# Performance work log

Measured on AMD Instinct MI355X. Metric: run time of the kernel, lower is better.

Reference implementation:

```python
import jax, jax.numpy as jnp
import numpy as np

B, CIN, COUT, G = 1, 64, 64, 1
NLAT, NLON = 256, 512
LMAX, MMAX = NLAT, NLON // 2 + 1  # torch-harmonics: lmax=nlat, mmax=nlon//2+1


def _legpoly(mmax, lmax, cost):
    """Fully (ortho) normalized associated Legendre \bar P_l^m(cos t), shape [mmax, lmax, nlat]."""
    nlat = cost.shape[0]
    p = np.zeros((mmax, lmax, nlat), dtype=np.float64)
    sint = np.sqrt(1.0 - cost * cost)
    pmm = np.full(nlat, np.sqrt(1.0 / (4.0 * np.pi)))  # \bar P_0^0
    for m in range(mmax):
        if m < lmax:
            p[m, m] = pmm
        if m + 1 < lmax:
            p[m, m + 1] = np.sqrt(2.0 * m + 3.0) * cost * pmm
        for l in range(m + 2, lmax):
            a = np.sqrt((4.0 * l * l - 1.0) / (l * l - m * m))
            b = np.sqrt(((l - 1.0) ** 2 - m * m) / (4.0 * (l - 1.0) ** 2 - 1.0))
            p[m, l] = a * (cost * p[m, l - 1] - b * p[m, l - 2])
        # diagonal step: \bar P_{m+1}^{m+1}
        pmm = -np.sqrt((2.0 * m + 3.0) / (2.0 * m + 2.0)) * sint * pmm
    return p


def setup_inputs():
    key = jax.random.key(0)
    k1, k2, k3 = jax.random.split(key, 3)
    # Gauss-Legendre nodes/weights (grid='legendre-gauss')
    cost, wq = np.polynomial.legendre.leggauss(NLAT)
    pct = _legpoly(MMAX, LMAX, cost)                      # [m, l, k] - ISHT matrix
    sht_w = pct * wq[None, None, :]                        # [m, l, k] - SHT matrix (Legendre * quadrature)
    x = jax.random.normal(k1, (B, CIN, NLAT, NLON), jnp.float32)
    # weight init: scale = sqrt(1/(Cin/g)), scale[0] *= sqrt(2); complex randn has var 1/2 per component
    scale = np.full(LMAX, np.sqrt(1.0 / (CIN // G)), np.float32)
    scale[0] *= np.sqrt(2.0)
    scale = scale * np.sqrt(0.5)
    weight_r = jax.random.normal(k2, (G, CIN // G, COUT // G, LMAX), jnp.float32) * scale
    weight_i = jax.random.normal(k3, (G, CIN // G, COUT // G, LMAX), jnp.float32) * scale
    return {"x": x, "weight_r": weight_r, "weight_i": weight_i,
            "pct": jnp.asarray(pct.astype(np.float32)),
            "sht_w": jnp.asarray(sht_w.astype(np.float32))}


def reference(x, weight_r, weight_i, pct, sht_w):
    residual = x  # scale_residual is False (same in/out shape and grid)
    x = x.astype(jnp.float32)
    # --- forward real SHT: rfft over lon, Legendre transform over lat ---
    xf = 2.0 * jnp.pi * jnp.fft.rfft(x, axis=-1, norm="forward")          # [B,C,k,m] complex64
    coeffs = jnp.einsum('bckm,mlk->bclm', xf, sht_w.astype(xf.dtype))      # [B,C,l,m]
    Bd, C, L, M = coeffs.shape
    # --- grouped per-l complex weight contraction (_contract_lwise) ---
    w = (weight_r + 1j * weight_i).astype(coeffs.dtype)                    # [g,i,o,l]
    xg = coeffs.reshape(Bd, G, C // G, L, M)
    out = jnp.einsum('bgilm,giol->bgolm', xg, w).reshape(Bd, COUT, L, M)
    # --- inverse real SHT ---
    xk = jnp.einsum('bolm,mlk->bokm', out, pct.astype(out.dtype))          # [B,Cout,k,m]
    y = jnp.fft.irfft(xk, n=NLON, axis=-1, norm="forward")                 # [B,Cout,nlat,nlon]
    return (y.astype(residual.dtype), residual)
```

## Files before the change

kernel.cpp:

```cpp
#include <hip/hip_runtime.h>

typedef _Float16 f16;
typedef _Float16 h8 __attribute__((ext_vector_type(8)));
typedef float f4 __attribute__((ext_vector_type(4)));

#define NLON 512
#define NLAT 256
#define NC   64
#define NM   256
#define NL   256
#define RTOT (NC*NLAT)

#define BO_FTR 0
#define BO_FTI (BO_FTR + 262144)
#define BO_GR  (BO_FTI + 262144)
#define BO_GI  (BO_GR  + 262144)
#define BO_WTR (BO_GI  + 262144)
#define BO_WTI (BO_WTR + 2097152)
#define BO_XFRE (BO_WTI + 2097152)
#define BO_XFIM (BO_XFRE + 8388608)
#define BO_PRE  (BO_XFIM + 8388608)
#define BO_PIM  (BO_PRE + 8388608)
#define BO_QRE  (BO_PIM + 8388608)
#define BO_QIM  (BO_QRE + 8388608)

__device__ inline f4 mfma16(h8 a, h8 b, f4 c) {
  return __builtin_amdgcn_mfma_f32_16x16x32_f16(a, b, c, 0, 0, 0);
}

__global__ void k_tables_h(f16* __restrict__ Ftr, f16* __restrict__ Fti,
                           f16* __restrict__ Gr, f16* __restrict__ Gi) {
  int idx = blockIdx.x * blockDim.x + threadIdx.x;
  if (idx >= NLON * NM) return;
  const float step = 3.14159265358979323846f / 256.0f;
  {
    int m = idx >> 9, n = idx & 511;
    int t = (n * m) & (NLON - 1);
    float th = t * step;
    const float sc = 6.2831853071795864769f / 512.0f;
    Ftr[idx] = (f16)(sc * cosf(th));
    Fti[idx] = (f16)(-sc * sinf(th));
  }
  {
    int n = idx >> 8, m = idx & 255;
    int t = (n * m) & (NLON - 1);
    float th = t * step;
    float s = (m == 0) ? 1.0f : 2.0f;
    Gr[idx] = (f16)(s * cosf(th));
    Gi[idx] = (f16)(-s * sinf(th));
  }
}

__global__ void k_permw2(const float* __restrict__ wr, const float* __restrict__ wi,
                         f16* __restrict__ wTr, f16* __restrict__ wTi) {
  __shared__ float tile[32][33];
  int z = blockIdx.z;
  int o = z >> 1;
  const float* w = (z & 1) ? wi : wr;
  f16* wT = (z & 1) ? wTi : wTr;
  int i0 = blockIdx.y * 32;
  int l0 = blockIdx.x * 32;
  int xx = threadIdx.x, yy = threadIdx.y;
  for (int j = 0; j < 32; j += 8)
    tile[yy + j][xx] = w[(size_t)(i0 + yy + j) * (NC * NL) + (size_t)o * NL + l0 + xx];
  __syncthreads();
  for (int j = 0; j < 32; j += 8)
    wT[(size_t)(l0 + yy + j) * (NC * NC) + (size_t)o * NC + i0 + xx] = (f16)tile[xx][yy + j];
}

__global__ __launch_bounds__(256) void k_s1(
    const float* __restrict__ x, const f16* __restrict__ Ftr,
    const f16* __restrict__ Fti, f16* __restrict__ XFre, f16* __restrict__ XFim,
    float* __restrict__ res) {
  __shared__ f16 Ar[64 * 40], Ai[64 * 40], Bx[64 * 40];
  int t = threadIdx.x;
  int m0 = blockIdx.x * 64, r0 = blockIdx.y * 64;
  int lane = t & 63, w = t >> 6;
  int wm = (w >> 1) * 32, wn = (w & 1) * 32;
  int fr = lane & 15, kg = (lane >> 4) * 8;
  int srow = t >> 2, skc = (t & 3) * 8;
  f4 aR[2][2] = {}, aI[2][2] = {};
  for (int n0 = 0; n0 < NLON; n0 += 32) {
    *(h8*)&Ar[srow * 40 + skc] = *(const h8*)(Ftr + (size_t)(m0 + srow) * NLON + n0 + skc);
    *(h8*)&Ai[srow * 40 + skc] = *(const h8*)(Fti + (size_t)(m0 + srow) * NLON + n0 + skc);
    const float* px = x + (size_t)(r0 + srow) * NLON + n0 + skc;
    float4 v0 = *(const float4*)px;
    float4 v1 = *(const float4*)(px + 4);
    if (blockIdx.x == 0) {
      float* pr = res + (size_t)(r0 + srow) * NLON + n0 + skc;
      *(float4*)pr = v0;
      *(float4*)(pr + 4) = v1;
    }
    h8 hx = {(f16)v0.x, (f16)v0.y, (f16)v0.z, (f16)v0.w,
             (f16)v1.x, (f16)v1.y, (f16)v1.z, (f16)v1.w};
    *(h8*)&Bx[srow * 40 + skc] = hx;
    __syncthreads();
    h8 a0 = *(h8*)&Ar[(wm + fr) * 40 + kg];
    h8 a1 = *(h8*)&Ar[(wm + 16 + fr) * 40 + kg];
    h8 c0 = *(h8*)&Ai[(wm + fr) * 40 + kg];
    h8 c1 = *(h8*)&Ai[(wm + 16 + fr) * 40 + kg];
    h8 b0 = *(h8*)&Bx[(wn + fr) * 40 + kg];
    h8 b1 = *(h8*)&Bx[(wn + 16 + fr) * 40 + kg];
    aR[0][0] = mfma16(a0, b0, aR[0][0]); aR[0][1] = mfma16(a0, b1, aR[0][1]);
    aR[1][0] = mfma16(a1, b0, aR[1][0]); aR[1][1] = mfma16(a1, b1, aR[1][1]);
    aI[0][0] = mfma16(c0, b0, aI[0][0]); aI[0][1] = mfma16(c0, b1, aI[0][1]);
    aI[1][0] = mfma16(c1, b0, aI[1][0]); aI[1][1] = mfma16(c1, b1, aI[1][1]);
    __syncthreads();
  }
  int drow = (lane >> 4) * 4, dcol = lane & 15;
#pragma unroll
  for (int i = 0; i < 2; ++i)
#pragma unroll
    for (int j = 0; j < 2; ++j)
#pragma unroll
      for (int b = 0; b < 4; ++b) {
        size_t o = (size_t)(m0 + wm + i * 16 + drow + b) * RTOT + r0 + wn + j * 16 + dcol;
        XFre[o] = (f16)aR[i][j][b];
        XFim[o] = (f16)aI[i][j][b];
      }
}

__global__ __launch_bounds__(256) void k_s2(
    const f16* __restrict__ XFre, const f16* __restrict__ XFim,
    const float* __restrict__ shtw, f16* __restrict__ Pre, f16* __restrict__ Pim) {
  int m = blockIdx.y;
  int l0 = blockIdx.x * 64;
  int t = threadIdx.x;
  if (l0 + 64 <= m) {
    h8 z = {};
#pragma unroll
    for (int rep = 0; rep < 2; ++rep) {
      int f = rep * 256 + t;
      int ll = f >> 3, c8 = (f & 7) * 8;
      size_t o = (size_t)(l0 + ll) * RTOT + (size_t)m * 64 + c8;
      *(h8*)(Pre + o) = z;
      *(h8*)(Pim + o) = z;
    }
    return;
  }
  __shared__ f16 SH[9216];
  f16* Ar = SH;
  f16* Ai = SH + 2560;
  f16* Bs = SH + 5120;
  int lane = t & 63, w = t >> 6;
  int wm = (w >> 1) * 32, wn = (w & 1) * 32;
  int fr = lane & 15, kg = (lane >> 4) * 8;
  int srow = t >> 2, skc = (t & 3) * 8;
  const f16* Abr = XFre + (size_t)m * RTOT;
  const f16* Abi = XFim + (size_t)m * RTOT;
  const float* Bb = shtw + (size_t)m * (NL * NLAT);
  f4 aR[2][2] = {}, aI[2][2] = {};
  for (int k0 = 0; k0 < NLAT; k0 += 32) {
    *(h8*)&Ar[srow * 40 + skc] = *(const h8*)(Abr + (size_t)srow * NLAT + k0 + skc);
    *(h8*)&Ai[srow * 40 + skc] = *(const h8*)(Abi + (size_t)srow * NLAT + k0 + skc);
    const float* pb = Bb + (size_t)(l0 + srow) * NLAT + k0 + skc;
    float4 v0 = *(const float4*)pb;
    float4 v1 = *(const float4*)(pb + 4);
    h8 hb = {(f16)v0.x, (f16)v0.y, (f16)v0.z, (f16)v0.w,
             (f16)v1.x, (f16)v1.y, (f16)v1.z, (f16)v1.w};
    *(h8*)&Bs[srow * 40 + skc] = hb;
    __syncthreads();
    h8 a0 = *(h8*)&Ar[(wm + fr) * 40 + kg],      a1 = *(h8*)&Ar[(wm + 16 + fr) * 40 + kg];
    h8 c0 = *(h8*)&Ai[(wm + fr) * 40 + kg],      c1 = *(h8*)&Ai[(wm + 16 + fr) * 40 + kg];
    h8 b0 = *(h8*)&Bs[(wn + fr) * 40 + kg],      b1 = *(h8*)&Bs[(wn + 16 + fr) * 40 + kg];
    aR[0][0] = mfma16(a0, b0, aR[0][0]); aR[0][1] = mfma16(a0, b1, aR[0][1]);
    aR[1][0] = mfma16(a1, b0, aR[1][0]); aR[1][1] = mfma16(a1, b1, aR[1][1]);
    aI[0][0] = mfma16(c0, b0, aI[0][0]); aI[0][1] = mfma16(c0, b1, aI[0][1]);
    aI[1][0] = mfma16(c1, b0, aI[1][0]); aI[1][1] = mfma16(c1, b1, aI[1][1]);
    __syncthreads();
  }
  f16* Tr = SH;
  f16* Ti = SH + 4608;
  int drow = (lane >> 4) * 4, dcol = lane & 15;
#pragma unroll
  for (int i = 0; i < 2; ++i)
#pragma unroll
    for (int j = 0; j < 2; ++j)
#pragma unroll
      for (int b = 0; b < 4; ++b) {
        int c = wm + i * 16 + drow + b;
        int l = wn + j * 16 + dcol;
        Tr[l * 72 + c] = (f16)aR[i][j][b];
        Ti[l * 72 + c] = (f16)aI[i][j][b];
      }
  __syncthreads();
#pragma unroll
  for (int rep = 0; rep < 4; ++rep) {
    int f = rep * 256 + t;
    int buf = f >> 9, idx = f & 511;
    int ll = idx >> 3, c8 = (idx & 7) * 8;
    const f16* T = buf ? Ti : Tr;
    h8 v = *(const h8*)&T[ll * 72 + c8];
    f16* Pd = buf ? Pim : Pre;
    *(h8*)(Pd + (size_t)(l0 + ll) * RTOT + (size_t)m * 64 + c8) = v;
  }
}

__global__ __launch_bounds__(256) void k_s3(
    const f16* __restrict__ Pre, const f16* __restrict__ Pim,
    const f16* __restrict__ wTr, const f16* __restrict__ wTi,
    f16* __restrict__ Qre, f16* __restrict__ Qim) {
  int l = blockIdx.y;
  int m0 = blockIdx.x * 64;
  int t = threadIdx.x;
  size_t obase = (size_t)l * RTOT + (size_t)m0 * 64;
  if (m0 > l) {
    h8 z = {};
#pragma unroll
    for (int rep = 0; rep < 2; ++rep) {
      int f = rep * 256 + t;
      ((h8*)(Qre + obase))[f] = z;
      ((h8*)(Qim + obase))[f] = z;
    }
    return;
  }
  __shared__ f16 SH[18432];
  f16* Ar = SH;
  f16* Ai = SH + 4608;
  f16* Br = SH + 9216;
  f16* Bi = SH + 13824;
  const f16* Pbr = Pre + (size_t)l * RTOT + (size_t)m0 * 64;
  const f16* Pbi = Pim + (size_t)l * RTOT + (size_t)m0 * 64;
  const f16* Wbr = wTr + (size_t)l * 4096;
  const f16* Wbi = wTi + (size_t)l * 4096;
#pragma unroll
  for (int rep = 0; rep < 2; ++rep) {
    int f = rep * 256 + t;
    int row = f >> 3, c8 = (f & 7) * 8;
    *(h8*)&Ar[row * 72 + c8] = *(const h8*)(Pbr + (size_t)row * 64 + c8);
    *(h8*)&Ai[row * 72 + c8] = *(const h8*)(Pbi + (size_t)row * 64 + c8);
    *(h8*)&Br[row * 72 + c8] = *(const h8*)(Wbr + (size_t)f * 8);
    *(h8*)&Bi[row * 72 + c8] = *(const h8*)(Wbi + (size_t)f * 8);
  }
  __syncthreads();
  int lane = t & 63, w = t >> 6;
  int wm = (w >> 1) * 32, wn = (w & 1) * 32;
  int fr = lane & 15, kg = (lane >> 4) * 8;
  f4 RR[2][2] = {}, II[2][2] = {}, RI[2][2] = {}, IR[2][2] = {};
#pragma unroll
  for (int ks = 0; ks < 64; ks += 32) {
    h8 a0 = *(h8*)&Ar[(wm + fr) * 72 + ks + kg];
    h8 a1 = *(h8*)&Ar[(wm + 16 + fr) * 72 + ks + kg];
    h8 c0 = *(h8*)&Ai[(wm + fr) * 72 + ks + kg];
    h8 c1 = *(h8*)&Ai[(wm + 16 + fr) * 72 + ks + kg];
    h8 b0 = *(h8*)&Br[(wn + fr) * 72 + ks + kg];
    h8 b1 = *(h8*)&Br[(wn + 16 + fr) * 72 + ks + kg];
    h8 d0 = *(h8*)&Bi[(wn + fr) * 72 + ks + kg];
    h8 d1 = *(h8*)&Bi[(wn + 16 + fr) * 72 + ks + kg];
    RR[0][0] = mfma16(a0, b0, RR[0][0]); RR[0][1] = mfma16(a0, b1, RR[0][1]);
    RR[1][0] = mfma16(a1, b0, RR[1][0]); RR[1][1] = mfma16(a1, b1, RR[1][1]);
    II[0][0] = mfma16(c0, d0, II[0][0]); II[0][1] = mfma16(c0, d1, II[0][1]);
    II[1][0] = mfma16(c1, d0, II[1][0]); II[1][1] = mfma16(c1, d1, II[1][1]);
    RI[0][0] = mfma16(a0, d0, RI[0][0]); RI[0][1] = mfma16(a0, d1, RI[0][1]);
    RI[1][0] = mfma16(a1, d0, RI[1][0]); RI[1][1] = mfma16(a1, d1, RI[1][1]);
    IR[0][0] = mfma16(c0, b0, IR[0][0]); IR[0][1] = mfma16(c0, b1, IR[0][1]);
    IR[1][0] = mfma16(c1, b0, IR[1][0]); IR[1][1] = mfma16(c1, b1, IR[1][1]);
  }
  __syncthreads();
  f16* Tr = SH;
  f16* Ti = SH + 4608;
  int drow = (lane >> 4) * 4, dcol = lane & 15;
#pragma unroll
  for (int i = 0; i < 2; ++i)
#pragma unroll
    for (int j = 0; j < 2; ++j)
#pragma unroll
      for (int b = 0; b < 4; ++b) {
        int mm = wm + i * 16 + drow + b;
        int oo = wn + j * 16 + dcol;
        Tr[mm * 72 + oo] = (f16)(RR[i][j][b] - II[i][j][b]);
        Ti[mm * 72 + oo] = (f16)(RI[i][j][b] + IR[i][j][b]);
      }
  __syncthreads();
#pragma unroll
  for (int rep = 0; rep < 4; ++rep) {
    int f = rep * 256 + t;
    int buf = f >> 9, idx = f & 511;
    int mm = idx >> 3, o8 = (idx & 7) * 8;
    const f16* T = buf ? Ti : Tr;
    h8 v = *(const h8*)&T[mm * 72 + o8];
    f16* Qd = buf ? Qim : Qre;
    *(h8*)(Qd + obase + (size_t)mm * 64 + o8) = v;
  }
}

__global__ __launch_bounds__(256) void k_s4(
    const f16* __restrict__ Qre, const f16* __restrict__ Qim,
    const float* __restrict__ pct, f16* __restrict__ XKre, f16* __restrict__ XKim) {
  __shared__ f16 As[32 * 66], Ais[32 * 66], Bs0[32 * 66], Bs1[32 * 66];
  int m = blockIdx.y;
  int k0b = blockIdx.x * 128;
  int t = threadIdx.x;
  int lane = t & 63, w = t >> 6;
  int wm = (w >> 1) * 32, wn = (w & 1) * 32;
  int fr = lane & 15, kg = (lane >> 4) * 8;
  int lr = t >> 3, c8 = (t & 7) * 8;
  const float* Bb = pct + (size_t)m * (NL * NLAT);
  f4 aR[2][4] = {}, aI[2][4] = {};
  int lstart = m & ~31;
  for (int l0 = lstart; l0 < NL; l0 += 32) {
    *(h8*)&As[lr * 66 + c8]  = *(const h8*)(Qre + (size_t)(l0 + lr) * RTOT + (size_t)m * 64 + c8);
    *(h8*)&Ais[lr * 66 + c8] = *(const h8*)(Qim + (size_t)(l0 + lr) * RTOT + (size_t)m * 64 + c8);
    const float* pb = Bb + (size_t)(l0 + lr) * NLAT + k0b + c8;
    {
      float4 v0 = *(const float4*)pb;
      float4 v1 = *(const float4*)(pb + 4);
      h8 hb = {(f16)v0.x, (f16)v0.y, (f16)v0.z, (f16)v0.w,
               (f16)v1.x, (f16)v1.y, (f16)v1.z, (f16)v1.w};
      *(h8*)&Bs0[lr * 66 + c8] = hb;
    }
    {
      float4 v0 = *(const float4*)(pb + 64);
      float4 v1 = *(const float4*)(pb + 68);
      h8 hb = {(f16)v0.x, (f16)v0.y, (f16)v0.z, (f16)v0.w,
               (f16)v1.x, (f16)v1.y, (f16)v1.z, (f16)v1.w};
      *(h8*)&Bs1[lr * 66 + c8] = hb;
    }
    __syncthreads();
    h8 a0, a1, c0, c1, b0, b1, b2, b3;
#pragma unroll
    for (int e = 0; e < 8; ++e) {
      int row = (kg + e) * 66;
      a0[e] = As[row + wm + fr];
      a1[e] = As[row + wm + 16 + fr];
      c0[e] = Ais[row + wm + fr];
      c1[e] = Ais[row + wm + 16 + fr];
      b0[e] = Bs0[row + wn + fr];
      b1[e] = Bs0[row + wn + 16 + fr];
      b2[e] = Bs1[row + wn + fr];
      b3[e] = Bs1[row + wn + 16 + fr];
    }
    aR[0][0] = mfma16(a0, b0, aR[0][0]); aR[0][1] = mfma16(a0, b1, aR[0][1]);
    aR[0][2] = mfma16(a0, b2, aR[0][2]); aR[0][3] = mfma16(a0, b3, aR[0][3]);
    aR[1][0] = mfma16(a1, b0, aR[1][0]); aR[1][1] = mfma16(a1, b1, aR[1][1]);
    aR[1][2] = mfma16(a1, b2, aR[1][2]); aR[1][3] = mfma16(a1, b3, aR[1][3]);
    aI[0][0] = mfma16(c0, b0, aI[0][0]); aI[0][1] = mfma16(c0, b1, aI[0][1]);
    aI[0][2] = mfma16(c0, b2, aI[0][2]); aI[0][3] = mfma16(c0, b3, aI[0][3]);
    aI[1][0] = mfma16(c1, b0, aI[1][0]); aI[1][1] = mfma16(c1, b1, aI[1][1]);
    aI[1][2] = mfma16(c1, b2, aI[1][2]); aI[1][3] = mfma16(c1, b3, aI[1][3]);
    __syncthreads();
  }
  int drow = (lane >> 4) * 4, dcol = lane & 15;
#pragma unroll
  for (int i = 0; i < 2; ++i)
#pragma unroll
    for (int j = 0; j < 4; ++j)
#pragma unroll
      for (int b = 0; b < 4; ++b) {
        int orow = wm + i * 16 + drow + b;
        int kcol = k0b + (j >> 1) * 64 + (j & 1) * 16 + wn + dcol;
        size_t o = (size_t)m * RTOT + (size_t)orow * NLAT + kcol;
        XKre[o] = (f16)aR[i][j][b];
        XKim[o] = (f16)aI[i][j][b];
      }
}

__global__ __launch_bounds__(256) void k_s5(
    const f16* __restrict__ XKre, const f16* __restrict__ XKim,
    const f16* __restrict__ Gr, const f16* __restrict__ Gi,
    float* __restrict__ y) {
  __shared__ f16 Ar[32 * 66], Ai[32 * 66], Br[128 * 34], Bi[128 * 34];
  int t = threadIdx.x;
  int n0 = blockIdx.x * 128, r0 = blockIdx.y * 64;
  int lane = t & 63, w = t >> 6;
  int wm = (w >> 1) * 32, wn = (w & 1) * 32;
  int fr = lane & 15, kg = (lane >> 4) * 8;
  int mr = t >> 3, r8 = (t & 7) * 8;
  f4 acc[2][4] = {};
  for (int m0 = 0; m0 < NM; m0 += 32) {
    *(h8*)&Ar[mr * 66 + r8] = *(const h8*)(XKre + (size_t)(m0 + mr) * RTOT + r0 + r8);
    *(h8*)&Ai[mr * 66 + r8] = *(const h8*)(XKim + (size_t)(m0 + mr) * RTOT + r0 + r8);
#pragma unroll
    for (int rep = 0; rep < 2; ++rep) {
      int f = rep * 256 + t;
      int row = f >> 2, cc = (f & 3) * 8;
      *(h8*)&Br[row * 34 + cc] = *(const h8*)(Gr + (size_t)(n0 + row) * NM + m0 + cc);
      *(h8*)&Bi[row * 34 + cc] = *(const h8*)(Gi + (size_t)(n0 + row) * NM + m0 + cc);
    }
    __syncthreads();
    h8 a0, a1, c0, c1;
#pragma unroll
    for (int e = 0; e < 8; ++e) {
      int row = (kg + e) * 66;
      a0[e] = Ar[row + wm + fr];
      a1[e] = Ar[row + wm + 16 + fr];
      c0[e] = Ai[row + wm + fr];
      c1[e] = Ai[row + wm + 16 + fr];
    }
#pragma unroll
    for (int j = 0; j < 4; ++j) {
      int nb = wn + (j & 1) * 16 + (j >> 1) * 64;
      h8 b = *(h8*)&Br[(nb + fr) * 34 + kg];
      h8 d = *(h8*)&Bi[(nb + fr) * 34 + kg];
      acc[0][j] = mfma16(a0, b, acc[0][j]);
      acc[1][j] = mfma16(a1, b, acc[1][j]);
      acc[0][j] = mfma16(c0, d, acc[0][j]);
      acc[1][j] = mfma16(c1, d, acc[1][j]);
    }
    __syncthreads();
  }
  int drow = (lane >> 4) * 4, dcol = lane & 15;
#pragma unroll
  for (int i = 0; i < 2; ++i)
#pragma unroll
    for (int j = 0; j < 4; ++j)
#pragma unroll
      for (int b = 0; b < 4; ++b) {
        int rg = r0 + wm + i * 16 + drow + b;
        int ng = n0 + wn + (j & 1) * 16 + (j >> 1) * 64 + dcol;
        y[(size_t)rg * NLON + ng] = acc[i][j][b];
      }
}

extern "C" void kernel_launch(void* const* d_in, const int* in_sizes, int n_in,
                              void* d_out, int out_size, void* d_ws, size_t ws_size,
                              hipStream_t stream) {
  const float* x    = (const float*)d_in[0];
  const float* wgr  = (const float*)d_in[1];
  const float* wgi  = (const float*)d_in[2];
  const float* pct  = (const float*)d_in[3];
  const float* shtw = (const float*)d_in[4];
  float* out = (float*)d_out;
  char* ws = (char*)d_ws;

  f16* Ftr = (f16*)(ws + BO_FTR);
  f16* Fti = (f16*)(ws + BO_FTI);
  f16* Gr  = (f16*)(ws + BO_GR);
  f16* Gi  = (f16*)(ws + BO_GI);
  f16* wTr = (f16*)(ws + BO_WTR);
  f16* wTi = (f16*)(ws + BO_WTI);
  f16* XFre = (f16*)(ws + BO_XFRE);
  f16* XFim = (f16*)(ws + BO_XFIM);
  f16* Pre  = (f16*)(ws + BO_PRE);
  f16* Pim  = (f16*)(ws + BO_PIM);
  f16* Qre  = (f16*)(ws + BO_QRE);
  f16* Qim  = (f16*)(ws + BO_QIM);

  float* res = out + (size_t)NC * NLAT * NLON;

  hipLaunchKernelGGL(k_tables_h, dim3(512), dim3(256), 0, stream, Ftr, Fti, Gr, Gi);
  hipLaunchKernelGGL(k_permw2, dim3(8, 2, 128), dim3(32, 8), 0, stream, wgr, wgi, wTr, wTi);
  hipLaunchKernelGGL(k_s1, dim3(4, 256), dim3(256), 0, stream, x, Ftr, Fti, XFre, XFim, res);
  hipLaunchKernelGGL(k_s2, dim3(4, 256), dim3(256), 0, stream, XFre, XFim, shtw, Pre, Pim);
  hipLaunchKernelGGL(k_s3, dim3(4, 256), dim3(256), 0, stream, Pre, Pim, wTr, wTi, Qre, Qim);
  hipLaunchKernelGGL(k_s4, dim3(2, 256), dim3(256), 0, stream, Qre, Qim, pct, XFre, XFim);
  hipLaunchKernelGGL(k_s5, dim3(4, 256), dim3(256), 0, stream, XFre, XFim, Gr, Gi, out);
}
```

Before: 137.0 us.

## Double block size in forward DFT and inverse Legendre kernels with 8 warps

k_s1 now uses 512-thread blocks covering 128 output frequencies, so each x tile is loaded and converted once for twice as many m values. This halves redundant reads of the input across blocks, and the residual copy is split across the two blocks. k_s4 moves to 8 warps where each warp computes half the previous output tile, and the A and B tile loads are split between the two thread halves. Both changes raise per-block thread count and may lower per-warp register pressure, at the cost of fewer blocks in flight.

```diff
diff --git a/kernel.cpp b/kernel.cpp
--- a/kernel.cpp
+++ b/kernel.cpp
@@ -2,6 +2,7 @@
 
 typedef _Float16 f16;
 typedef _Float16 h8 __attribute__((ext_vector_type(8)));
+typedef _Float16 h4 __attribute__((ext_vector_type(4)));
 typedef float f4 __attribute__((ext_vector_type(4)));
 
 #define NLON 512
@@ -68,32 +69,29 @@
     wT[(size_t)(l0 + yy + j) * (NC * NC) + (size_t)o * NC + i0 + xx] = (f16)tile[xx][yy + j];
 }
 
-__global__ __launch_bounds__(256) void k_s1(
+__global__ __launch_bounds__(512) void k_s1(
     const float* __restrict__ x, const f16* __restrict__ Ftr,
     const f16* __restrict__ Fti, f16* __restrict__ XFre, f16* __restrict__ XFim,
     float* __restrict__ res) {
-  __shared__ f16 Ar[64 * 40], Ai[64 * 40], Bx[64 * 40];
+  __shared__ f16 Ar[128 * 40], Ai[128 * 40], Bx[64 * 40];
   int t = threadIdx.x;
-  int m0 = blockIdx.x * 64, r0 = blockIdx.y * 64;
+  int m0 = blockIdx.x * 128, r0 = blockIdx.y * 64;
   int lane = t & 63, w = t >> 6;
   int wm = (w >> 1) * 32, wn = (w & 1) * 32;
   int fr = lane & 15, kg = (lane >> 4) * 8;
-  int srow = t >> 2, skc = (t & 3) * 8;
+  int srowF = t >> 2, scF = (t & 3) * 8;
+  int rowX = t >> 3, colX = (t & 7) * 4;
   f4 aR[2][2] = {}, aI[2][2] = {};
   for (int n0 = 0; n0 < NLON; n0 += 32) {
-    *(h8*)&Ar[srow * 40 + skc] = *(const h8*)(Ftr + (size_t)(m0 + srow) * NLON + n0 + skc);
-    *(h8*)&Ai[srow * 40 + skc] = *(const h8*)(Fti + (size_t)(m0 + srow) * NLON + n0 + skc);
-    const float* px = x + (size_t)(r0 + srow) * NLON + n0 + skc;
-    float4 v0 = *(const float4*)px;
-    float4 v1 = *(const float4*)(px + 4);
-    if (blockIdx.x == 0) {
-      float* pr = res + (size_t)(r0 + srow) * NLON + n0 + skc;
-      *(float4*)pr = v0;
-      *(float4*)(pr + 4) = v1;
-    }
-    h8 hx = {(f16)v0.x, (f16)v0.y, (f16)v0.z, (f16)v0.w,
-             (f16)v1.x, (f16)v1.y, (f16)v1.z, (f16)v1.w};
-    *(h8*)&Bx[srow * 40 + skc] = hx;
+    *(h8*)&Ar[srowF * 40 + scF] = *(const h8*)(Ftr + (size_t)(m0 + srowF) * NLON + n0 + scF);
+    *(h8*)&Ai[srowF * 40 + scF] = *(const h8*)(Fti + (size_t)(m0 + srowF) * NLON + n0 + scF);
+    const float* px = x + (size_t)(r0 + rowX) * NLON + n0 + colX;
+    float4 v = *(const float4*)px;
+    if ((n0 >> 8) == blockIdx.x) {
+      *(float4*)(res + (size_t)(r0 + rowX) * NLON + n0 + colX) = v;
+    }
+    h4 hx = {(f16)v.x, (f16)v.y, (f16)v.z, (f16)v.w};
+    *(h4*)&Bx[rowX * 40 + colX] = hx;
     __syncthreads();
     h8 a0 = *(h8*)&Ar[(wm + fr) * 40 + kg];
     h8 a1 = *(h8*)&Ar[(wm + 16 + fr) * 40 + kg];
@@ -114,7 +112,8 @@
     for (int j = 0; j < 2; ++j)
 #pragma unroll
       for (int b = 0; b < 4; ++b) {
-        size_t o = (size_t)(m0 + wm + i * 16 + drow + b) * RTOT + r0 + wn + j * 16 + dcol;
+        int mg = m0 + wm + i * 16 + drow + b;
+        size_t o = (size_t)mg * RTOT + r0 + wn + j * 16 + dcol;
         XFre[o] = (f16)aR[i][j][b];
         XFim[o] = (f16)aI[i][j][b];
       }
@@ -284,7 +283,7 @@
   }
 }
 
-__global__ __launch_bounds__(256) void k_s4(
+__global__ __launch_bounds__(512) void k_s4(
     const f16* __restrict__ Qre, const f16* __restrict__ Qim,
     const float* __restrict__ pct, f16* __restrict__ XKre, f16* __restrict__ XKim) {
   __shared__ f16 As[32 * 66], Ais[32 * 66], Bs0[32 * 66], Bs1[32 * 66];
@@ -292,32 +291,40 @@
   int k0b = blockIdx.x * 128;
   int t = threadIdx.x;
   int lane = t & 63, w = t >> 6;
-  int wm = (w >> 1) * 32, wn = (w & 1) * 32;
+  int wm = (w >> 2) * 32;
+  int wn = (w & 3) * 32;
   int fr = lane & 15, kg = (lane >> 4) * 8;
-  int lr = t >> 3, c8 = (t & 7) * 8;
+  bool loA = t < 256;
+  int u = loA ? t : (t - 256);
+  int lr = u >> 3;
+  int c8 = (u & 7) * 8;
+  int kc = (u & 7) * 16;
   const float* Bb = pct + (size_t)m * (NL * NLAT);
-  f4 aR[2][4] = {}, aI[2][4] = {};
+  f4 aR[2][2] = {}, aI[2][2] = {};
   int lstart = m & ~31;
+  const f16* Bsel = (wn < 64) ? Bs0 : Bs1;
+  int wnl = wn & 63;
   for (int l0 = lstart; l0 < NL; l0 += 32) {
-    *(h8*)&As[lr * 66 + c8]  = *(const h8*)(Qre + (size_t)(l0 + lr) * RTOT + (size_t)m * 64 + c8);
-    *(h8*)&Ais[lr * 66 + c8] = *(const h8*)(Qim + (size_t)(l0 + lr) * RTOT + (size_t)m * 64 + c8);
-    const float* pb = Bb + (size_t)(l0 + lr) * NLAT + k0b + c8;
-    {
+    if (loA) {
+      *(h8*)&As[lr * 66 + c8]  = *(const h8*)(Qre + (size_t)(l0 + lr) * RTOT + (size_t)m * 64 + c8);
+      *(h8*)&Ais[lr * 66 + c8] = *(const h8*)(Qim + (size_t)(l0 + lr) * RTOT + (size_t)m * 64 + c8);
+    } else {
+      const float* pb = Bb + (size_t)(l0 + lr) * NLAT + k0b + kc;
       float4 v0 = *(const float4*)pb;
       float4 v1 = *(const float4*)(pb + 4);
-      h8 hb = {(f16)v0.x, (f16)v0.y, (f16)v0.z, (f16)v0.w,
+      float4 v2 = *(const float4*)(pb + 8);
+      float4 v3 = *(const float4*)(pb + 12);
+      h8 h0 = {(f16)v0.x, (f16)v0.y, (f16)v0.z, (f16)v0.w,
                (f16)v1.x, (f16)v1.y, (f16)v1.z, (f16)v1.w};
-      *(h8*)&Bs0[lr * 66 + c8] = hb;
-    }
-    {
-      float4 v0 = *(const float4*)(pb + 64);
-      float4 v1 = *(const float4*)(pb + 68);
-      h8 hb = {(f16)v0.x, (f16)v0.y, (f16)v0.z, (f16)v0.w,
-               (f16)v1.x, (f16)v1.y, (f16)v1.z, (f16)v1.w};
-      *(h8*)&Bs1[lr * 66 + c8] = hb;
-    }
-    __syncthreads();
-    h8 a0, a1, c0, c1, b0, b1, b2, b3;
+      h8 h1 = {(f16)v2.x, (f16)v2.y, (f16)v2.z, (f16)v2.w,
+               (f16)v3.x, (f16)v3.y, (f16)v3.z, (f16)v3.w};
+      f16* B = (kc < 64) ? Bs0 : Bs1;
+      int kl = kc & 63;
+      *(h8*)&B[lr * 66 + kl] = h0;
+      *(h8*)&B[lr * 66 + kl + 8] = h1;
+    }
+    __syncthreads();
+    h8 a0, a1, c0, c1, b0, b1;
 #pragma unroll
     for (int e = 0; e < 8; ++e) {
       int row = (kg + e) * 66;
@@ -325,30 +332,24 @@
       a1[e] = As[row + wm + 16 + fr];
       c0[e] = Ais[row + wm + fr];
       c1[e] = Ais[row + wm + 16 + fr];
-      b0[e] = Bs0[row + wn + fr];
-      b1[e] = Bs0[row + wn + 16 + fr];
-      b2[e] = Bs1[row + wn + fr];
-      b3[e] = Bs1[row + wn + 16 + fr];
+      b0[e] = Bsel[row + wnl + fr];
+      b1[e] = Bsel[row + wnl + 16 + fr];
     }
     aR[0][0] = mfma16(a0, b0, aR[0][0]); aR[0][1] = mfma16(a0, b1, aR[0][1]);
-    aR[0][2] = mfma16(a0, b2, aR[0][2]); aR[0][3] = mfma16(a0, b3, aR[0][3]);
     aR[1][0] = mfma16(a1, b0, aR[1][0]); aR[1][1] = mfma16(a1, b1, aR[1][1]);
-    aR[1][2] = mfma16(a1, b2, aR[1][2]); aR[1][3] = mfma16(a1, b3, aR[1][3]);
     aI[0][0] = mfma16(c0, b0, aI[0][0]); aI[0][1] = mfma16(c0, b1, aI[0][1]);
-    aI[0][2] = mfma16(c0, b2, aI[0][2]); aI[0][3] = mfma16(c0, b3, aI[0][3]);
     aI[1][0] = mfma16(c1, b0, aI[1][0]); aI[1][1] = mfma16(c1, b1, aI[1][1]);
-    aI[1][2] = mfma16(c1, b2, aI[1][2]); aI[1][3] = mfma16(c1, b3, aI[1][3]);
     __syncthreads();
   }
   int drow = (lane >> 4) * 4, dcol = lane & 15;
 #pragma unroll
   for (int i = 0; i < 2; ++i)
 #pragma unroll
-    for (int j = 0; j < 4; ++j)
+    for (int j = 0; j < 2; ++j)
 #pragma unroll
       for (int b = 0; b < 4; ++b) {
         int orow = wm + i * 16 + drow + b;
-        int kcol = k0b + (j >> 1) * 64 + (j & 1) * 16 + wn + dcol;
+        int kcol = k0b + wn + j * 16 + dcol;
         size_t o = (size_t)m * RTOT + (size_t)orow * NLAT + kcol;
         XKre[o] = (f16)aR[i][j][b];
         XKim[o] = (f16)aI[i][j][b];
@@ -440,9 +441,9 @@
 
   hipLaunchKernelGGL(k_tables_h, dim3(512), dim3(256), 0, stream, Ftr, Fti, Gr, Gi);
   hipLaunchKernelGGL(k_permw2, dim3(8, 2, 128), dim3(32, 8), 0, stream, wgr, wgi, wTr, wTi);
-  hipLaunchKernelGGL(k_s1, dim3(4, 256), dim3(256), 0, stream, x, Ftr, Fti, XFre, XFim, res);
+  hipLaunchKernelGGL(k_s1, dim3(2, 256), dim3(512), 0, stream, x, Ftr, Fti, XFre, XFim, res);
   hipLaunchKernelGGL(k_s2, dim3(4, 256), dim3(256), 0, stream, XFre, XFim, shtw, Pre, Pim);
   hipLaunchKernelGGL(k_s3, dim3(4, 256), dim3(256), 0, stream, Pre, Pim, wTr, wTi, Qre, Qim);
-  hipLaunchKernelGGL(k_s4, dim3(2, 256), dim3(256), 0, stream, Qre, Qim, pct, XFre, XFim);
+  hipLaunchKernelGGL(k_s4, dim3(2, 256), dim3(512), 0, stream, Qre, Qim, pct, XFre, XFim);
   hipLaunchKernelGGL(k_s5, dim3(4, 256), dim3(256), 0, stream, XFre, XFim, Gr, Gi, out);
 }
```

Result: faster. 118.0 us (-13.9%).
